# Kernel tuning notes

Measured on AMD Instinct MI355X. Metric: run time of the kernel, lower is better.

## Reference

```python
import jax, jax.numpy as jnp
import numpy as np

B, N, T_IN, F_IN = 16, 30000, 6, 1
E = 120000          # edges per etype
N_ETYPES = 2        # etypes per graph (hg and tg each)
KT, LK = 3, 3
C1, C2 = 8, 11      # block channel sizes
HID = 128


def _conv2d(x, w, b):
    # x: [B,Cin,T,N], w: [Cout,Cin,kt,1] -> valid conv
    y = jax.lax.conv_general_dilated(x, w, window_strides=(1, 1), padding='VALID',
                                     dimension_numbers=('NCHW', 'OIHW', 'NCHW'))
    return y + b[None, :, None, None]


def _glu_tconv(x, w, b, c_out, x_align):
    # TemporalConvLayer with act='GLU'
    xc = _conv2d(x, w, b)
    return (xc[:, :c_out] + x_align) * jax.nn.sigmoid(xc[:, c_out:])


def _hetcheb(X, edges, W, bias):
    # Heterogeneous ChebConv (sum over edge types), lambda_max=2 => L_hat = -D^-1/2 A D^-1/2
    # X: [S,N,Cin], edges: [n_et,2,E] int32, W: [n_et,Lk,Cin,Cout], bias: [n_et,Cout]
    S, n, cin = X.shape
    Lk = W.shape[1]
    Xn = jnp.transpose(X, (1, 0, 2))  # [N,S,Cin]
    out = jnp.zeros((n, S, W.shape[-1]), X.dtype)
    for e in range(edges.shape[0]):
        src, dst = edges[e, 0], edges[e, 1]
        ones = jnp.ones(src.shape, X.dtype)
        deg_in = jnp.clip(jax.ops.segment_sum(ones, dst, num_segments=n), 1.0)
        deg_out = jnp.clip(jax.ops.segment_sum(ones, src, num_segments=n), 1.0)
        norm = jax.lax.rsqrt(deg_out)[src] * jax.lax.rsqrt(deg_in)[dst]  # [E]
        def prop(Tm):  # L_hat @ T = -(Ahat @ T); vectorized over all B*T slices at once
            Tf = Tm.reshape(n, S * cin)
            return -jax.ops.segment_sum(norm[:, None] * Tf[src], dst, num_segments=n).reshape(n, S, cin)
        Tkm2 = Xn
        Tkm1 = prop(Xn)
        z = jnp.einsum('nsc,cd->nsd', Tkm2, W[e, 0]) + jnp.einsum('nsc,cd->nsd', Tkm1, W[e, 1])
        for k in range(2, Lk):
            Tk = 2.0 * prop(Tkm1) - Tkm2
            z = z + jnp.einsum('nsc,cd->nsd', Tk, W[e, k])
            Tkm2, Tkm1 = Tkm1, Tk
        out = out + z + bias[e][None, None, :]
    return jnp.transpose(out, (1, 0, 2))  # [S,N,Cout]


def _block(x, hg_edges, tg_edges, align_fn, tw, tb, hW, hb, tW, tb2, c_out):
    # HetETAConvBlock (dropout = identity in eval)
    x_align = align_fn(x)[:, :, KT - 1:, :]
    x_t1 = _glu_tconv(x, tw, tb, c_out, x_align)          # [B,c_out,T',N]
    b_, c_, t_, n_ = x_t1.shape
    X = jnp.transpose(x_t1, (0, 2, 3, 1)).reshape(b_ * t_, n_, c_)  # batched slices
    xs = _hetcheb(X, hg_edges, hW, hb).reshape(b_, t_, n_, -1).transpose(0, 3, 1, 2)
    xt = _hetcheb(X, tg_edges, tW, tb2).reshape(b_, t_, n_, -1).transpose(0, 3, 1, 2)
    return jnp.concatenate([xs, xt], axis=1)              # [B,2*c_out,T',N]


def setup_inputs() -> dict:
    key = jax.random.key(0)
    ks = jax.random.split(key, 20)
    s = 0.1
    inp = {
        'x': jax.random.normal(ks[0], (B, N, T_IN, F_IN), jnp.float32),
        'hg_edges': jax.random.randint(ks[1], (N_ETYPES, 2, E), 0, N, jnp.int32),
        'tg_edges': jax.random.randint(ks[2], (N_ETYPES, 2, E), 0, N, jnp.int32),
        # block1: tconv GLU 1 -> 8 (out 2*8 channels)
        'tconv1_w': jax.random.normal(ks[3], (2 * C1, F_IN, KT, 1), jnp.float32) * s,
        'tconv1_b': jnp.zeros((2 * C1,), jnp.float32),
        'h1_W': jax.random.normal(ks[4], (N_ETYPES, LK, C1, C1), jnp.float32) * s,
        'h1_b': jnp.zeros((N_ETYPES, C1), jnp.float32),
        't1_W': jax.random.normal(ks[5], (N_ETYPES, LK, C1, C1), jnp.float32) * s,
        't1_b': jnp.zeros((N_ETYPES, C1), jnp.float32),
        # block2: align 16 -> 11 (conv1x1), tconv GLU 16 -> 11
        'align2_w': jax.random.normal(ks[6], (C2, 2 * C1, 1, 1), jnp.float32) * s,
        'align2_b': jnp.zeros((C2,), jnp.float32),
        'tconv2_w': jax.random.normal(ks[7], (2 * C2, 2 * C1, KT, 1), jnp.float32) * s,
        'tconv2_b': jnp.zeros((2 * C2,), jnp.float32),
        'h2_W': jax.random.normal(ks[8], (N_ETYPES, LK, C2, C2), jnp.float32) * s,
        'h2_b': jnp.zeros((N_ETYPES, C2), jnp.float32),
        't2_W': jax.random.normal(ks[9], (N_ETYPES, LK, C2, C2), jnp.float32) * s,
        't2_b': jnp.zeros((N_ETYPES, C2), jnp.float32),
        # output linear: 11*2*(6-2*(3-1)) = 44 -> HID
        'out_w': jax.random.normal(ks[10], (2 * C2 * (T_IN - 2 * (KT - 1)), HID), jnp.float32) * s,
        'out_b': jnp.zeros((HID,), jnp.float32),
    }
    return inp


def reference(x, hg_edges, tg_edges, tconv1_w, tconv1_b, h1_W, h1_b, t1_W, t1_b,
              align2_w, align2_b, tconv2_w, tconv2_b, h2_W, h2_b, t2_W, t2_b,
              out_w, out_b):
    x = jnp.transpose(x, (0, 3, 2, 1))  # [B,1,T,N]
    # block1: Align pads channels 1 -> 8
    align1 = lambda v: jnp.pad(v, ((0, 0), (0, C1 - F_IN), (0, 0), (0, 0)))
    x1 = _block(x, hg_edges, tg_edges, align1, tconv1_w, tconv1_b, h1_W, h1_b, t1_W, t1_b, C1)
    # block2: Align is 1x1 conv 16 -> 11
    align2 = lambda v: _conv2d(v, align2_w, align2_b)
    x2 = _block(x1, hg_edges, tg_edges, align2, tconv2_w, tconv2_b, h2_W, h2_b, t2_W, t2_b, C2)
    b_, c_, t_, n_ = x2.shape
    z = jnp.transpose(x2, (0, 3, 1, 2)).reshape(b_, n_, c_ * t_)  # [B,N,44]
    return z @ out_w + out_b  # [B,N,HID]
```

## Files before the change

### kernel.cpp

```cpp
#include <hip/hip_runtime.h>
#include <hip/hip_fp16.h>
#include <math.h>

#define EDGES 120000
#define NN    30000
#define NCH   118
#define T1SLOT 15360000

__device__ __forceinline__ float sigmoidf_(float x) { return 1.f / (1.f + __expf(-x)); }

union F4H8 { float4 v; __half h[8]; };
union F2H4 { float2 v; __half h[4]; };

__device__ __forceinline__ void unpack8(float4 v, float* f) {
  F4H8 u; u.v = v;
#pragma unroll
  for (int i = 0; i < 8; ++i) f[i] = __half2float(u.h[i]);
}
__device__ __forceinline__ float4 pack8(const float* f) {
  F4H8 u;
#pragma unroll
  for (int i = 0; i < 8; ++i) u.h[i] = __float2half(f[i]);
  return u.v;
}
__device__ __forceinline__ void unpack4(float2 v, float* f) {
  F2H4 u; u.v = v;
#pragma unroll
  for (int i = 0; i < 4; ++i) f[i] = __half2float(u.h[i]);
}
__device__ __forceinline__ float2 pack4(const float* f) {
  F2H4 u;
#pragma unroll
  for (int i = 0; i < 4; ++i) u.h[i] = __float2half(f[i]);
  return u.v;
}

#define CSR_STRIDE 270016
#define CSR_RP(base, l)   ((base) + (size_t)(l) * CSR_STRIDE)
#define CSR_PK(base, l)   ((const int2*)((base) + (size_t)(l) * CSR_STRIDE + 30016))
#define CSR_PKW(base, l)  ((int2*)((base) + (size_t)(l) * CSR_STRIDE + 30016))

__global__ void count_all_kernel(const int* __restrict__ hg, const int* __restrict__ tg,
                                 int* __restrict__ degO, int* __restrict__ degI) {
  int tid = blockIdx.x * blockDim.x + threadIdx.x;
  if (tid >= 4 * EDGES) return;
  int l = tid / EDGES, j = tid - l * EDGES;
  const int* G = (l < 2) ? hg : tg;
  const int* src = G + (size_t)(l & 1) * 2 * EDGES;
  const int* dst = src + EDGES;
  atomicAdd(&degO[l * NN + src[j]], 1);
  atomicAdd(&degI[l * NN + dst[j]], 1);
}

__global__ __launch_bounds__(256) void scan1_kernel(const int* __restrict__ degI,
                                                    int* __restrict__ csrBase,
                                                    int* __restrict__ partials) {
  int l = blockIdx.x / NCH, ch = blockIdx.x - l * NCH;
  int tid = threadIdx.x;
  int i = ch * 256 + tid;
  __shared__ int buf[256];
  int v = (i < NN) ? degI[l * NN + i] : 0;
  buf[tid] = v;
  __syncthreads();
  for (int off = 1; off < 256; off <<= 1) {
    int t = (tid >= off) ? buf[tid - off] : 0;
    __syncthreads();
    buf[tid] += t;
    __syncthreads();
  }
  int* rp = CSR_RP(csrBase, l);
  if (i < NN) rp[i + 1] = buf[tid];
  if (tid == 255) partials[l * NCH + ch] = buf[255];
}

__global__ __launch_bounds__(128) void scan2_kernel(int* __restrict__ partials) {
  __shared__ int buf[128];
  int tid = threadIdx.x;
  for (int l = 0; l < 4; ++l) {
    int v = (tid < NCH) ? partials[l * NCH + tid] : 0;
    buf[tid] = v;
    __syncthreads();
    for (int off = 1; off < 128; off <<= 1) {
      int t = (tid >= off) ? buf[tid - off] : 0;
      __syncthreads();
      buf[tid] += t;
      __syncthreads();
    }
    if (tid < NCH) partials[l * NCH + tid] = buf[tid] - v;
    __syncthreads();
  }
}

__global__ __launch_bounds__(256) void fixup_kernel(int* __restrict__ csrBase,
                                                    int* __restrict__ cursor,
                                                    const int* __restrict__ partials) {
  int l = blockIdx.x / NCH, ch = blockIdx.x - l * NCH;
  int i = ch * 256 + threadIdx.x;
  int* rp = CSR_RP(csrBase, l);
  int off = partials[l * NCH + ch];
  if (i < NN) {
    int val = rp[i + 1] + off;
    rp[i + 1] = val;
    if (i + 1 < NN) cursor[l * NN + i + 1] = val;
  }
  if (i == 0) { rp[0] = 0; cursor[l * NN] = 0; }
}

__global__ void fill_all_kernel(const int* __restrict__ hg, const int* __restrict__ tg,
                                const int* __restrict__ degO, const int* __restrict__ degI,
                                int* __restrict__ cursor, int* __restrict__ csrBase) {
  int tid = blockIdx.x * blockDim.x + threadIdx.x;
  if (tid >= 4 * EDGES) return;
  int l = tid / EDGES, j = tid - l * EDGES;
  const int* G = (l < 2) ? hg : tg;
  const int* src = G + (size_t)(l & 1) * 2 * EDGES;
  const int* dst = src + EDGES;
  int s = src[j], d = dst[j];
  int doo = degO[l * NN + s]; if (doo < 1) doo = 1;
  int dii = degI[l * NN + d]; if (dii < 1) dii = 1;
  float nm = rsqrtf((float)doo) * rsqrtf((float)dii);
  int p = atomicAdd(&cursor[l * NN + d], 1);
  CSR_PKW(csrBase, l)[p] = make_int2(s, __float_as_int(nm));
}

__global__ void glu1_kernel(const float* __restrict__ x, const float* __restrict__ w,
                            const float* __restrict__ b, __half* __restrict__ X1h) {
  int idx = blockIdx.x * blockDim.x + threadIdx.x;
  if (idx >= NN * 64) return;
  int n = idx >> 6, s = idx & 63;
  int bb = s >> 2, t = s & 3;
  const float* xb = x + ((long)bb * NN + n) * 6;
  float x0 = xb[t], x1 = xb[t + 1], x2 = xb[t + 2];
  float o[8];
#pragma unroll
  for (int c = 0; c < 8; ++c) {
    float p = w[c * 3 + 0] * x0 + w[c * 3 + 1] * x1 + w[c * 3 + 2] * x2 + b[c];
    float q = w[(c + 8) * 3 + 0] * x0 + w[(c + 8) * 3 + 1] * x1 + w[(c + 8) * 3 + 2] * x2 + b[c + 8];
    float al = (c == 0) ? x2 : 0.f;
    o[c] = (p + al) * sigmoidf_(q);
  }
  reinterpret_cast<float4*>(X1h)[idx] = pack8(o);
}

__global__ __launch_bounds__(256) void pull1_kernel(const int* __restrict__ csrBase,
                                                    const __half* __restrict__ Xh,
                                                    __half* __restrict__ T1hAll) {
  int gtid = blockIdx.x * 256 + threadIdx.x;
  int l = gtid / (NN * 64);
  int t = gtid - l * (NN * 64);
  int n = t >> 6, j = t & 63;
  const int* rp = CSR_RP(csrBase, l);
  const int2* pk = CSR_PK(csrBase, l);
  const float4* in4 = reinterpret_cast<const float4*>(Xh);
  float acc[8];
#pragma unroll
  for (int i = 0; i < 8; ++i) acc[i] = 0.f;
  int e = rp[n], end = rp[n + 1];
  for (; e + 4 <= end; e += 4) {
    int2 p0 = pk[e], p1 = pk[e + 1], p2 = pk[e + 2], p3 = pk[e + 3];
    float4 v0 = in4[(long)p0.x * 64 + j];
    float4 v1 = in4[(long)p1.x * 64 + j];
    float4 v2 = in4[(long)p2.x * 64 + j];
    float4 v3 = in4[(long)p3.x * 64 + j];
    float f[8];
    float n0 = __int_as_float(p0.y), n1 = __int_as_float(p1.y);
    float n2 = __int_as_float(p2.y), n3 = __int_as_float(p3.y);
    unpack8(v0, f);
#pragma unroll
    for (int i = 0; i < 8; ++i) acc[i] -= n0 * f[i];
    unpack8(v1, f);
#pragma unroll
    for (int i = 0; i < 8; ++i) acc[i] -= n1 * f[i];
    unpack8(v2, f);
#pragma unroll
    for (int i = 0; i < 8; ++i) acc[i] -= n2 * f[i];
    unpack8(v3, f);
#pragma unroll
    for (int i = 0; i < 8; ++i) acc[i] -= n3 * f[i];
  }
  for (; e < end; ++e) {
    int2 p = pk[e];
    float4 v = in4[(long)p.x * 64 + j];
    float nm = __int_as_float(p.y);
    float f[8];
    unpack8(v, f);
#pragma unroll
    for (int i = 0; i < 8; ++i) acc[i] -= nm * f[i];
  }
  reinterpret_cast<float4*>(T1hAll)[(size_t)l * (T1SLOT / 8) + t] = pack8(acc);
}

__global__ __launch_bounds__(256) void cheb1_kernel(const int* __restrict__ csrBase,
    const __half* __restrict__ Xh, const __half* __restrict__ T1hAll,
    const float* __restrict__ Whg, const float* __restrict__ bhg,
    const float* __restrict__ Wtg, const float* __restrict__ btg,
    __half* __restrict__ outH, __half* __restrict__ outT) {
  constexpr int C = 8, CC = 64;
  __shared__ float wx[CC], w1a[CC], w1b[CC], w2a[CC], w2b[CC], bs[C];
  int gtid = blockIdx.x * 256 + threadIdx.x;
  int g = gtid / (NN * 64);
  int tid = gtid - g * (NN * 64);
  const float* W = g ? Wtg : Whg;
  const float* bias = g ? btg : bhg;
  for (int i = threadIdx.x; i < CC; i += 256) {
    float w0A = W[i], w1A = W[CC + i], w2A = W[2 * CC + i];
    float w0B = W[3 * CC + i], w1B = W[4 * CC + i], w2B = W[5 * CC + i];
    wx[i] = w0A - w2A + w0B - w2B;
    w1a[i] = w1A; w1b[i] = w1B;
    w2a[i] = -2.f * w2A; w2b[i] = -2.f * w2B;
  }
  if (threadIdx.x < C) bs[threadIdx.x] = bias[threadIdx.x] + bias[C + threadIdx.x];
  __syncthreads();
  int n = tid >> 6, s = tid & 63;
  int l0 = 2 * g, l1 = 2 * g + 1;
  const int* rp0 = CSR_RP(csrBase, l0); const int2* pk0 = CSR_PK(csrBase, l0);
  const int* rp1 = CSR_RP(csrBase, l1); const int2* pk1 = CSR_PK(csrBase, l1);
  const float4* A4 = reinterpret_cast<const float4*>(T1hAll + (size_t)l0 * T1SLOT);
  const float4* B4 = reinterpret_cast<const float4*>(T1hAll + (size_t)l1 * T1SLOT);
  float acc0[C], acc1[C];
#pragma unroll
  for (int c = 0; c < C; ++c) { acc0[c] = 0.f; acc1[c] = 0.f; }
  {
    int e = rp0[n], end = rp0[n + 1];
    for (; e + 2 <= end; e += 2) {
      int2 p0 = pk0[e], p1 = pk0[e + 1];
      float4 v0 = A4[(long)p0.x * 64 + s];
      float4 v1 = A4[(long)p1.x * 64 + s];
      float n0 = __int_as_float(p0.y), n1 = __int_as_float(p1.y);
      float f0[8], f1[8];
      unpack8(v0, f0); unpack8(v1, f1);
#pragma unroll
      for (int c = 0; c < C; ++c) acc0[c] += n0 * f0[c] + n1 * f1[c];
    }
    for (; e < end; ++e) {
      int2 p = pk0[e];
      float4 v = A4[(long)p.x * 64 + s];
      float nm = __int_as_float(p.y);
      float f[8]; unpack8(v, f);
#pragma unroll
      for (int c = 0; c < C; ++c) acc0[c] += nm * f[c];
    }
  }
  {
    int e = rp1[n], end = rp1[n + 1];
    for (; e + 2 <= end; e += 2) {
      int2 p0 = pk1[e], p1 = pk1[e + 1];
      float4 v0 = B4[(long)p0.x * 64 + s];
      float4 v1 = B4[(long)p1.x * 64 + s];
      float n0 = __int_as_float(p0.y), n1 = __int_as_float(p1.y);
      float f0[8], f1[8];
      unpack8(v0, f0); unpack8(v1, f1);
#pragma unroll
      for (int c = 0; c < C; ++c) acc1[c] += n0 * f0[c] + n1 * f1[c];
    }
    for (; e < end; ++e) {
      int2 p = pk1[e];
      float4 v = B4[(long)p.x * 64 + s];
      float nm = __int_as_float(p.y);
      float f[8]; unpack8(v, f);
#pragma unroll
      for (int c = 0; c < C; ++c) acc1[c] += nm * f[c];
    }
  }
  float z[C];
#pragma unroll
  for (int d = 0; d < C; ++d) z[d] = bs[d];
  {
    float xv[8], av[8], bv[8];
    unpack8(reinterpret_cast<const float4*>(Xh)[tid], xv);
    unpack8(A4[tid], av);
    unpack8(B4[tid], bv);
#pragma unroll
    for (int c = 0; c < C; ++c) {
      float x0c = xv[c], tac = av[c], tbc = bv[c], a0 = acc0[c], a1 = acc1[c];
#pragma unroll
      for (int d = 0; d < C; ++d)
        z[d] += x0c * wx[c * C + d] + tac * w1a[c * C + d] + tbc * w1b[c * C + d] +
                a0 * w2a[c * C + d] + a1 * w2b[c * C + d];
    }
  }
  reinterpret_cast<float4*>(g ? outT : outH)[tid] = pack8(z);
}

__global__ __launch_bounds__(256) void glu2_kernel(const __half* __restrict__ H, const __half* __restrict__ Tt,
                                                   const float* __restrict__ w2, const float* __restrict__ b2,
                                                   const float* __restrict__ aw, const float* __restrict__ ab,
                                                   __half* __restrict__ X2nh) {
  __shared__ float w2s[22 * 16 * 3], b2s[22], aws[11 * 16], abs_[11];
  for (int i = threadIdx.x; i < 22 * 16 * 3; i += 256) w2s[i] = w2[i];
  if (threadIdx.x < 22) b2s[threadIdx.x] = b2[threadIdx.x];
  for (int i = threadIdx.x; i < 11 * 16; i += 256) aws[i] = aw[i];
  if (threadIdx.x < 11) abs_[threadIdx.x] = ab[threadIdx.x];
  __syncthreads();
  int idx = blockIdx.x * 256 + threadIdx.x;
  int n = idx >> 5, s = idx & 31;
  int bb = s >> 1, t = s & 1;
  long rbase = (long)n * 64 + bb * 4 + t;
  const float4* H4 = reinterpret_cast<const float4*>(H) + rbase;
  const float4* T4 = reinterpret_cast<const float4*>(Tt) + rbase;
  float hv[24], tv[24];
  unpack8(H4[0], hv); unpack8(H4[1], hv + 8); unpack8(H4[2], hv + 16);
  unpack8(T4[0], tv); unpack8(T4[1], tv + 8); unpack8(T4[2], tv + 16);
  float o[12];
  o[11] = 0.f;
#pragma unroll
  for (int co = 0; co < 11; ++co) {
    float p = b2s[co], q = b2s[co + 11], a = abs_[co];
#pragma unroll
    for (int ci = 0; ci < 16; ++ci) {
      float v0 = (ci < 8) ? hv[ci] : tv[ci - 8];
      float v1 = (ci < 8) ? hv[8 + ci] : tv[ci];
      float v2 = (ci < 8) ? hv[16 + ci] : tv[8 + ci];
      p += w2s[(co * 16 + ci) * 3 + 0] * v0 + w2s[(co * 16 + ci) * 3 + 1] * v1 +
           w2s[(co * 16 + ci) * 3 + 2] * v2;
      q += w2s[((co + 11) * 16 + ci) * 3 + 0] * v0 + w2s[((co + 11) * 16 + ci) * 3 + 1] * v1 +
           w2s[((co + 11) * 16 + ci) * 3 + 2] * v2;
      a += aws[co * 16 + ci] * v2;
    }
    o[co] = (p + a) * sigmoidf_(q);
  }
  float2* o2 = reinterpret_cast<float2*>(X2nh) + (long)idx * 3;
  o2[0] = pack4(o);
  o2[1] = pack4(o + 4);
  o2[2] = pack4(o + 8);
}

__global__ __launch_bounds__(256) void pull2_kernel(const int* __restrict__ csrBase,
                                                    const __half* __restrict__ Xh,
                                                    __half* __restrict__ T1hAll) {
  int gtid = blockIdx.x * 256 + threadIdx.x;
  int l = gtid / (NN * 96);
  int t = gtid - l * (NN * 96);
  int n = t / 96, j = t - n * 96;
  const int* rp = CSR_RP(csrBase, l);
  const int2* pk = CSR_PK(csrBase, l);
  const float2* in2 = reinterpret_cast<const float2*>(Xh);
  float acc[4];
#pragma unroll
  for (int i = 0; i < 4; ++i) acc[i] = 0.f;
  int e = rp[n], end = rp[n + 1];
  for (; e + 4 <= end; e += 4) {
    int2 p0 = pk[e], p1 = pk[e + 1], p2 = pk[e + 2], p3 = pk[e + 3];
    float2 v0 = in2[(long)p0.x * 96 + j];
    float2 v1 = in2[(long)p1.x * 96 + j];
    float2 v2 = in2[(long)p2.x * 96 + j];
    float2 v3 = in2[(long)p3.x * 96 + j];
    float f[4];
    float n0 = __int_as_float(p0.y), n1 = __int_as_float(p1.y);
    float n2 = __int_as_float(p2.y), n3 = __int_as_float(p3.y);
    unpack4(v0, f);
#pragma unroll
    for (int i = 0; i < 4; ++i) acc[i] -= n0 * f[i];
    unpack4(v1, f);
#pragma unroll
    for (int i = 0; i < 4; ++i) acc[i] -= n1 * f[i];
    unpack4(v2, f);
#pragma unroll
    for (int i = 0; i < 4; ++i) acc[i] -= n2 * f[i];
    unpack4(v3, f);
#pragma unroll
    for (int i = 0; i < 4; ++i) acc[i] -= n3 * f[i];
  }
  for (; e < end; ++e) {
    int2 p = pk[e];
    float2 v = in2[(long)p.x * 96 + j];
    float nm = __int_as_float(p.y);
    float f[4];
    unpack4(v, f);
#pragma unroll
    for (int i = 0; i < 4; ++i) acc[i] -= nm * f[i];
  }
  reinterpret_cast<float2*>(T1hAll)[(size_t)l * (T1SLOT / 4) + t] = pack4(acc);
}

__global__ __launch_bounds__(256) void cheb2_kernel(const int* __restrict__ csrBase,
    const __half* __restrict__ Xh, const __half* __restrict__ T1hAll,
    const float* __restrict__ Whg, const float* __restrict__ bhg,
    const float* __restrict__ Wtg, const float* __restrict__ btg,
    __half* __restrict__ outH, __half* __restrict__ outT) {
  constexpr int C = 11, CC = 121;
  __shared__ float wx[CC], w1a[CC], w1b[CC], w2a[CC], w2b[CC], bs[C];
  int gtid = blockIdx.x * 256 + threadIdx.x;
  int g = gtid / (NN * 32);
  int tid = gtid - g * (NN * 32);
  const float* W = g ? Wtg : Whg;
  const float* bias = g ? btg : bhg;
  for (int i = threadIdx.x; i < CC; i += 256) {
    float w0A = W[i], w1A = W[CC + i], w2A = W[2 * CC + i];
    float w0B = W[3 * CC + i], w1B = W[4 * CC + i], w2B = W[5 * CC + i];
    wx[i] = w0A - w2A + w0B - w2B;
    w1a[i] = w1A; w1b[i] = w1B;
    w2a[i] = -2.f * w2A; w2b[i] = -2.f * w2B;
  }
  if (threadIdx.x < C) bs[threadIdx.x] = bias[threadIdx.x] + bias[C + threadIdx.x];
  __syncthreads();
  int n = tid >> 5, s = tid & 31;
  int s3 = s * 3;
  int l0 = 2 * g, l1 = 2 * g + 1;
  const int* rp0 = CSR_RP(csrBase, l0); const int2* pk0 = CSR_PK(csrBase, l0);
  const int* rp1 = CSR_RP(csrBase, l1); const int2* pk1 = CSR_PK(csrBase, l1);
  const float2* A2v = reinterpret_cast<const float2*>(T1hAll + (size_t)l0 * T1SLOT);
  const float2* B2v = reinterpret_cast<const float2*>(T1hAll + (size_t)l1 * T1SLOT);
// ... 42 lines not shown
      for (int i = 0; i < 4; ++i) acc0[4 + i] += nm * f[i];
      unpack4(a2, f);
#pragma unroll
      for (int i = 0; i < 4; ++i) acc0[8 + i] += nm * f[i];
    }
  }
  {
    int e = rp1[n], end = rp1[n + 1];
    for (; e + 2 <= end; e += 2) {
      int2 p0 = pk1[e], p1 = pk1[e + 1];
      long r0 = (long)p0.x * 96 + s3, r1 = (long)p1.x * 96 + s3;
      float2 a0 = B2v[r0], a1 = B2v[r0 + 1], a2 = B2v[r0 + 2];
      float2 b0 = B2v[r1], b1 = B2v[r1 + 1], b2 = B2v[r1 + 2];
      float n0 = __int_as_float(p0.y), n1 = __int_as_float(p1.y);
      float f[4];
      unpack4(a0, f);
#pragma unroll
      for (int i = 0; i < 4; ++i) acc1[i] += n0 * f[i];
      unpack4(a1, f);
#pragma unroll
      for (int i = 0; i < 4; ++i) acc1[4 + i] += n0 * f[i];
      unpack4(a2, f);
#pragma unroll
      for (int i = 0; i < 4; ++i) acc1[8 + i] += n0 * f[i];
      unpack4(b0, f);
#pragma unroll
      for (int i = 0; i < 4; ++i) acc1[i] += n1 * f[i];
      unpack4(b1, f);
#pragma unroll
      for (int i = 0; i < 4; ++i) acc1[4 + i] += n1 * f[i];
      unpack4(b2, f);
#pragma unroll
      for (int i = 0; i < 4; ++i) acc1[8 + i] += n1 * f[i];
    }
    for (; e < end; ++e) {
      int2 p = pk1[e];
      long r = (long)p.x * 96 + s3;
      float2 a0 = B2v[r], a1 = B2v[r + 1], a2 = B2v[r + 2];
      float nm = __int_as_float(p.y);
      float f[4];
      unpack4(a0, f);
#pragma unroll
      for (int i = 0; i < 4; ++i) acc1[i] += nm * f[i];
      unpack4(a1, f);
#pragma unroll
      for (int i = 0; i < 4; ++i) acc1[4 + i] += nm * f[i];
      unpack4(a2, f);
#pragma unroll
      for (int i = 0; i < 4; ++i) acc1[8 + i] += nm * f[i];
    }
  }
  float z[12];
#pragma unroll
  for (int d = 0; d < C; ++d) z[d] = bs[d];
  z[11] = 0.f;
  const float2* X2v = reinterpret_cast<const float2*>(Xh);
  long own = (long)tid * 3;
#pragma unroll
  for (int q = 0; q < 3; ++q) {
    float xv[4], av[4], bv[4];
    unpack4(X2v[own + q], xv);
    unpack4(A2v[own + q], av);
    unpack4(B2v[own + q], bv);
#pragma unroll
    for (int k = 0; k < 4; ++k) {
      int c = q * 4 + k;
      if (c == 11) continue;
      float x0c = xv[k], tac = av[k], tbc = bv[k], a0 = acc0[c], a1 = acc1[c];
#pragma unroll
      for (int d = 0; d < C; ++d)
        z[d] += x0c * wx[c * C + d] + tac * w1a[c * C + d] + tbc * w1b[c * C + d] +
                a0 * w2a[c * C + d] + a1 * w2b[c * C + d];
    }
  }
  float2* o2 = reinterpret_cast<float2*>(g ? outT : outH) + (long)tid * 3;
  o2[0] = pack4(z);
  o2[1] = pack4(z + 4);
  o2[2] = pack4(z + 8);
}

__global__ __launch_bounds__(256) void final_kernel(const __half* __restrict__ H2, const __half* __restrict__ T2b,
                                                    const float* __restrict__ W, const float* __restrict__ bias,
                                                    float* __restrict__ out) {
  __shared__ __half zsr[64][48];
  int tid = threadIdx.x;
  long r0 = (long)blockIdx.x * 64;
#pragma unroll
  for (int it = 0; it < 2; ++it) {
    int item = it * 256 + tid;
    if (item < 384) {
      int row = item / 6, piece = item - row * 6;
      long r = r0 + row;
      int b = (int)(r / NN), n = (int)(r - (long)b * NN);
      const float4* srcb = reinterpret_cast<const float4*>(piece < 3 ? H2 : T2b);
      int f4i = (piece < 3) ? piece : piece - 3;
      float4 v = srcb[(long)n * 48 + b * 3 + f4i];
      *reinterpret_cast<float4*>(&zsr[row][(piece < 3 ? 0 : 24) + f4i * 8]) = v;
    }
  }
  int c = tid & 127, h = tid >> 7;
  float wp[48];
#pragma unroll
  for (int off = 0; off < 48; ++off) {
    int half_ = off / 24, r_ = off - half_ * 24;
    int t = r_ / 12, c_ = r_ - t * 12;
    wp[off] = (c_ == 11) ? 0.f : W[(2 * (c_ + half_ * 11) + t) * 128 + c];
  }
  float bh = bias[c];
  __syncthreads();
  int rbeg = h * 32;
#pragma unroll 2
  for (int row = rbeg; row < rbeg + 32; ++row) {
    const float4* zr4 = reinterpret_cast<const float4*>(&zsr[row][0]);
    float acc = bh;
#pragma unroll
    for (int q = 0; q < 6; ++q) {
      F4H8 u; u.v = zr4[q];
#pragma unroll
      for (int i = 0; i < 8; ++i)
        acc = fmaf(__half2float(u.h[i]), wp[q * 8 + i], acc);
    }
    out[(r0 + row) * 128 + c] = acc;
  }
}

extern "C" void kernel_launch(void* const* d_in, const int* in_sizes, int n_in,
                              void* d_out, int out_size, void* d_ws, size_t ws_size,
                              hipStream_t stream) {
  const float* x    = (const float*)d_in[0];
  const int*   hg   = (const int*)d_in[1];
  const int*   tg   = (const int*)d_in[2];
  const float* t1w  = (const float*)d_in[3];
  const float* t1b  = (const float*)d_in[4];
  const float* h1W  = (const float*)d_in[5];
  const float* h1b  = (const float*)d_in[6];
  const float* g1W  = (const float*)d_in[7];
  const float* g1b  = (const float*)d_in[8];
  const float* a2w  = (const float*)d_in[9];
  const float* a2b  = (const float*)d_in[10];
  const float* t2w  = (const float*)d_in[11];
  const float* t2b  = (const float*)d_in[12];
  const float* h2W  = (const float*)d_in[13];
  const float* h2b  = (const float*)d_in[14];
  const float* g2W  = (const float*)d_in[15];
  const float* g2b  = (const float*)d_in[16];
  const float* outw = (const float*)d_in[17];
  const float* outb = (const float*)d_in[18];
  float* out = (float*)d_out;

  __half* T1h = (__half*)d_ws;
  __half* Xh  = T1h + 4L * T1SLOT;
  __half* Cfh = Xh + T1SLOT;
  __half* Dfh = Cfh + T1SLOT;
  int* csrBase  = (int*)(Dfh + T1SLOT);
  int* degO     = csrBase + 4 * CSR_STRIDE;
  int* degI     = degO + 4 * NN;
  int* cursor   = degI + 4 * NN;
  int* partials = cursor + 4 * NN;

  hipMemsetAsync(degO, 0, 8 * NN * sizeof(int), stream);
  count_all_kernel<<<(4 * EDGES + 255) / 256, 256, 0, stream>>>(hg, tg, degO, degI);
  scan1_kernel<<<4 * NCH, 256, 0, stream>>>(degI, csrBase, partials);
  scan2_kernel<<<1, 128, 0, stream>>>(partials);
  fixup_kernel<<<4 * NCH, 256, 0, stream>>>(csrBase, cursor, partials);
  fill_all_kernel<<<(4 * EDGES + 255) / 256, 256, 0, stream>>>(hg, tg, degO, degI, cursor, csrBase);

  glu1_kernel<<<NN * 64 / 256, 256, 0, stream>>>(x, t1w, t1b, Xh);
  pull1_kernel<<<4 * NN * 64 / 256, 256, 0, stream>>>(csrBase, Xh, T1h);
  cheb1_kernel<<<2 * NN * 64 / 256, 256, 0, stream>>>(csrBase, Xh, T1h, h1W, h1b, g1W, g1b, Cfh, Dfh);

  glu2_kernel<<<NN * 32 / 256, 256, 0, stream>>>(Cfh, Dfh, t2w, t2b, a2w, a2b, Xh);
  pull2_kernel<<<4 * NN * 96 / 256, 256, 0, stream>>>(csrBase, Xh, T1h);
  cheb2_kernel<<<2 * NN * 32 / 256, 256, 0, stream>>>(csrBase, Xh, T1h, h2W, h2b, g2W, g2b, Cfh, Dfh);

  final_kernel<<<7500, 256, 0, stream>>>(Cfh, Dfh, outw, outb, out);
}
```

Before: 831.1 us.

## Restructure block-1 Chebyshev layout per batch group with XCD-aware persistent scheduling

Changes the block-1 feature layout from node-major [N][B*T][C] to batch-major [B][N][T*C]. Each thread of the pull and cheb kernels now owns one node and one batch, accumulating 32 values per edge over contiguous 64-byte rows. The kernels use persistent blocks that map batches to XCDs (blockIdx & 7) so each XCD's L2 holds the gather source for its batches. Cheb1 now writes per-edge-type partials that glu2 sums, and stores use non-temporal hints. The final kernel becomes grid-stride and the workspace buffers are aliased. The risks are higher register pressure from 32 accumulators, more partial traffic, and reliance on the blockIdx-to-XCD mapping.

```diff
diff --git a/kernel.cpp b/kernel.cpp
--- a/kernel.cpp
+++ b/kernel.cpp
@@ -5,11 +5,13 @@
 #define EDGES 120000
 #define NN    30000
 #define NCH   118
+#define CHUNKS 118
 #define T1SLOT 15360000
 
 __device__ __forceinline__ float sigmoidf_(float x) { return 1.f / (1.f + __expf(-x)); }
 
-union F4H8 { float4 v; __half h[8]; };
+typedef float f4raw __attribute__((ext_vector_type(4)));
+union F4H8 { float4 v; f4raw r; __half h[8]; };
 union F2H4 { float2 v; __half h[4]; };
 
 __device__ __forceinline__ void unpack8(float4 v, float* f) {
@@ -32,6 +34,14 @@
   F2H4 u;
 #pragma unroll
   for (int i = 0; i < 4; ++i) u.h[i] = __float2half(f[i]);
+  return u.v;
+}
+__device__ __forceinline__ void nt_store4(float4* p, float4 v) {
+  F4H8 u; u.v = v;
+  __builtin_nontemporal_store(u.r, reinterpret_cast<f4raw*>(p));
+}
+__device__ __forceinline__ float4 nt_load4(const float4* p) {
+  F4H8 u; u.r = __builtin_nontemporal_load(reinterpret_cast<const f4raw*>(p));
   return u.v;
 }
 
@@ -123,166 +133,201 @@
   CSR_PKW(csrBase, l)[p] = make_int2(s, __float_as_int(nm));
 }
 
-__global__ void glu1_kernel(const float* __restrict__ x, const float* __restrict__ w,
-                            const float* __restrict__ b, __half* __restrict__ X1h) {
-  int idx = blockIdx.x * blockDim.x + threadIdx.x;
-  if (idx >= NN * 64) return;
-  int n = idx >> 6, s = idx & 63;
-  int bb = s >> 2, t = s & 3;
-  const float* xb = x + ((long)bb * NN + n) * 6;
-  float x0 = xb[t], x1 = xb[t + 1], x2 = xb[t + 2];
+__global__ __launch_bounds__(256) void glu1_kernel(const float* __restrict__ x, const float* __restrict__ w,
+                                                   const float* __restrict__ b, __half* __restrict__ X1p) {
+  int tid = blockIdx.x * 256 + threadIdx.x;
+  int q = tid & 3;
+  int gn = tid >> 2;
+  int g = gn / NN, n = gn - g * NN;
+  const float* xb = x + ((long)g * NN + n) * 6;
+  float x0 = xb[q], x1 = xb[q + 1], x2 = xb[q + 2];
   float o[8];
 #pragma unroll
   for (int c = 0; c < 8; ++c) {
     float p = w[c * 3 + 0] * x0 + w[c * 3 + 1] * x1 + w[c * 3 + 2] * x2 + b[c];
-    float q = w[(c + 8) * 3 + 0] * x0 + w[(c + 8) * 3 + 1] * x1 + w[(c + 8) * 3 + 2] * x2 + b[c + 8];
+    float qq = w[(c + 8) * 3 + 0] * x0 + w[(c + 8) * 3 + 1] * x1 + w[(c + 8) * 3 + 2] * x2 + b[c + 8];
     float al = (c == 0) ? x2 : 0.f;
-    o[c] = (p + al) * sigmoidf_(q);
-  }
-  reinterpret_cast<float4*>(X1h)[idx] = pack8(o);
+    o[c] = (p + al) * sigmoidf_(qq);
+  }
+  reinterpret_cast<float4*>(X1p)[tid] = pack8(o);
 }
 
 __global__ __launch_bounds__(256) void pull1_kernel(const int* __restrict__ csrBase,
-                                                    const __half* __restrict__ Xh,
-                                                    __half* __restrict__ T1hAll) {
-  int gtid = blockIdx.x * 256 + threadIdx.x;
-  int l = gtid / (NN * 64);
-  int t = gtid - l * (NN * 64);
-  int n = t >> 6, j = t & 63;
-  const int* rp = CSR_RP(csrBase, l);
-  const int2* pk = CSR_PK(csrBase, l);
-  const float4* in4 = reinterpret_cast<const float4*>(Xh);
-  float acc[8];
-#pragma unroll
-  for (int i = 0; i < 8; ++i) acc[i] = 0.f;
-  int e = rp[n], end = rp[n + 1];
-  for (; e + 4 <= end; e += 4) {
-    int2 p0 = pk[e], p1 = pk[e + 1], p2 = pk[e + 2], p3 = pk[e + 3];
-    float4 v0 = in4[(long)p0.x * 64 + j];
-    float4 v1 = in4[(long)p1.x * 64 + j];
-    float4 v2 = in4[(long)p2.x * 64 + j];
-    float4 v3 = in4[(long)p3.x * 64 + j];
-    float f[8];
-    float n0 = __int_as_float(p0.y), n1 = __int_as_float(p1.y);
-    float n2 = __int_as_float(p2.y), n3 = __int_as_float(p3.y);
-    unpack8(v0, f);
-#pragma unroll
-    for (int i = 0; i < 8; ++i) acc[i] -= n0 * f[i];
-    unpack8(v1, f);
-#pragma unroll
-    for (int i = 0; i < 8; ++i) acc[i] -= n1 * f[i];
-    unpack8(v2, f);
-#pragma unroll
-    for (int i = 0; i < 8; ++i) acc[i] -= n2 * f[i];
-    unpack8(v3, f);
-#pragma unroll
-    for (int i = 0; i < 8; ++i) acc[i] -= n3 * f[i];
-  }
-  for (; e < end; ++e) {
-    int2 p = pk[e];
-    float4 v = in4[(long)p.x * 64 + j];
-    float nm = __int_as_float(p.y);
-    float f[8];
-    unpack8(v, f);
-#pragma unroll
-    for (int i = 0; i < 8; ++i) acc[i] -= nm * f[i];
-  }
-  reinterpret_cast<float4*>(T1hAll)[(size_t)l * (T1SLOT / 8) + t] = pack8(acc);
+                                                    const __half* __restrict__ X1p,
+                                                    __half* __restrict__ T1p) {
+  int xcd = blockIdx.x & 7, bslot = blockIdx.x >> 3;
+  for (int it = bslot; it < 2 * 4 * CHUNKS; it += 256) {
+    int chunk = it % CHUNKS;
+    int li = it / CHUNKS;
+    int l = li & 3, gl = li >> 2;
+    int g = gl * 8 + xcd;
+    int n = chunk * 256 + threadIdx.x;
+    if (n >= NN) continue;
+    const int* rp = CSR_RP(csrBase, l);
+    const int2* pk = CSR_PK(csrBase, l);
+    const float4* Xp = reinterpret_cast<const float4*>(X1p) + (size_t)g * NN * 4;
+    float acc[32];
+#pragma unroll
+    for (int i = 0; i < 32; ++i) acc[i] = 0.f;
+    int e = rp[n], end = rp[n + 1];
+    for (; e + 2 <= end; e += 2) {
+      int2 p0 = pk[e], p1 = pk[e + 1];
+      const float4* r0 = Xp + (size_t)p0.x * 4;
+      const float4* r1 = Xp + (size_t)p1.x * 4;
+      float4 a0 = r0[0], a1 = r0[1], a2 = r0[2], a3 = r0[3];
+      float4 b0 = r1[0], b1 = r1[1], b2 = r1[2], b3 = r1[3];
+      float n0 = __int_as_float(p0.y), n1 = __int_as_float(p1.y);
+      float f[8];
+      unpack8(a0, f);
+#pragma unroll
+      for (int i = 0; i < 8; ++i) acc[i] -= n0 * f[i];
+      unpack8(a1, f);
+#pragma unroll
+      for (int i = 0; i < 8; ++i) acc[8 + i] -= n0 * f[i];
+      unpack8(a2, f);
+#pragma unroll
+      for (int i = 0; i < 8; ++i) acc[16 + i] -= n0 * f[i];
+      unpack8(a3, f);
+#pragma unroll
+      for (int i = 0; i < 8; ++i) acc[24 + i] -= n0 * f[i];
+      unpack8(b0, f);
+#pragma unroll
+      for (int i = 0; i < 8; ++i) acc[i] -= n1 * f[i];
+      unpack8(b1, f);
+#pragma unroll
+      for (int i = 0; i < 8; ++i) acc[8 + i] -= n1 * f[i];
+      unpack8(b2, f);
+#pragma unroll
+      for (int i = 0; i < 8; ++i) acc[16 + i] -= n1 * f[i];
+      unpack8(b3, f);
+#pragma unroll
+      for (int i = 0; i < 8; ++i) acc[24 + i] -= n1 * f[i];
+    }
+    for (; e < end; ++e) {
+      int2 p = pk[e];
+      const float4* r0 = Xp + (size_t)p.x * 4;
+      float nm = __int_as_float(p.y);
+      float f[8];
+#pragma unroll
+      for (int rqi = 0; rqi < 4; ++rqi) {
+        unpack8(r0[rqi], f);
+#pragma unroll
+        for (int i = 0; i < 8; ++i) acc[rqi * 8 + i] -= nm * f[i];
+      }
+    }
+    float4* dst = reinterpret_cast<float4*>(T1p) + ((size_t)(l * 16 + g) * NN + n) * 4;
+    nt_store4(dst + 0, pack8(acc));
+    nt_store4(dst + 1, pack8(acc + 8));
+    nt_store4(dst + 2, pack8(acc + 16));
+    nt_store4(dst + 3, pack8(acc + 24));
+  }
 }
 
 __global__ __launch_bounds__(256) void cheb1_kernel(const int* __restrict__ csrBase,
-    const __half* __restrict__ Xh, const __half* __restrict__ T1hAll,
+    const __half* __restrict__ X1p, const __half* __restrict__ T1p,
     const float* __restrict__ Whg, const float* __restrict__ bhg,
     const float* __restrict__ Wtg, const float* __restrict__ btg,
-    __half* __restrict__ outH, __half* __restrict__ outT) {
-  constexpr int C = 8, CC = 64;
-  __shared__ float wx[CC], w1a[CC], w1b[CC], w2a[CC], w2b[CC], bs[C];
-  int gtid = blockIdx.x * 256 + threadIdx.x;
-  int g = gtid / (NN * 64);
-  int tid = gtid - g * (NN * 64);
-  const float* W = g ? Wtg : Whg;
-  const float* bias = g ? btg : bhg;
-  for (int i = threadIdx.x; i < CC; i += 256) {
-    float w0A = W[i], w1A = W[CC + i], w2A = W[2 * CC + i];
-    float w0B = W[3 * CC + i], w1B = W[4 * CC + i], w2B = W[5 * CC + i];
-    wx[i] = w0A - w2A + w0B - w2B;
-    w1a[i] = w1A; w1b[i] = w1B;
-    w2a[i] = -2.f * w2A; w2b[i] = -2.f * w2B;
-  }
-  if (threadIdx.x < C) bs[threadIdx.x] = bias[threadIdx.x] + bias[C + threadIdx.x];
-  __syncthreads();
-  int n = tid >> 6, s = tid & 63;
-  int l0 = 2 * g, l1 = 2 * g + 1;
-  const int* rp0 = CSR_RP(csrBase, l0); const int2* pk0 = CSR_PK(csrBase, l0);
-  const int* rp1 = CSR_RP(csrBase, l1); const int2* pk1 = CSR_PK(csrBase, l1);
-  const float4* A4 = reinterpret_cast<const float4*>(T1hAll + (size_t)l0 * T1SLOT);
-  const float4* B4 = reinterpret_cast<const float4*>(T1hAll + (size_t)l1 * T1SLOT);
-  float acc0[C], acc1[C];
-#pragma unroll
-  for (int c = 0; c < C; ++c) { acc0[c] = 0.f; acc1[c] = 0.f; }
-  {
-    int e = rp0[n], end = rp0[n + 1];
+    __half* __restrict__ P1) {
+  __shared__ float wx[64], w1[64], w2[64], bs[8];
+  int xcd = blockIdx.x & 7, bslot = blockIdx.x >> 3;
+  for (int it = bslot; it < 2 * 4 * CHUNKS; it += 256) {
+    int chunk = it % CHUNKS;
+    int li = it / CHUNKS;
+    int l = li & 3, gl = li >> 2;
+    int g = gl * 8 + xcd;
+    __syncthreads();
+    {
+      int grf = l >> 1, et = l & 1;
+      const float* W = (grf ? Wtg : Whg) + et * 3 * 64;
+      const float* bias = (grf ? btg : bhg) + et * 8;
+      for (int i = threadIdx.x; i < 64; i += 256) {
+        float w0v = W[i], w1v = W[64 + i], w2v = W[128 + i];
+        wx[i] = w0v - w2v; w1[i] = w1v; w2[i] = -2.f * w2v;
+      }
+      if (threadIdx.x < 8) bs[threadIdx.x] = bias[threadIdx.x];
+    }
+    __syncthreads();
+    int n = chunk * 256 + threadIdx.x;
+    if (n >= NN) continue;
+    const int* rp = CSR_RP(csrBase, l);
+    const int2* pk = CSR_PK(csrBase, l);
+    const float4* Tp = reinterpret_cast<const float4*>(T1p) + (size_t)(l * 16 + g) * NN * 4;
+    float acc[32];
+#pragma unroll
+    for (int i = 0; i < 32; ++i) acc[i] = 0.f;
+    int e = rp[n], end = rp[n + 1];
     for (; e + 2 <= end; e += 2) {
-      int2 p0 = pk0[e], p1 = pk0[e + 1];
-      float4 v0 = A4[(long)p0.x * 64 + s];
-      float4 v1 = A4[(long)p1.x * 64 + s];
+      int2 p0 = pk[e], p1 = pk[e + 1];
+      const float4* r0 = Tp + (size_t)p0.x * 4;
+      const float4* r1 = Tp + (size_t)p1.x * 4;
+      float4 a0 = r0[0], a1 = r0[1], a2 = r0[2], a3 = r0[3];
+      float4 b0 = r1[0], b1 = r1[1], b2 = r1[2], b3 = r1[3];
       float n0 = __int_as_float(p0.y), n1 = __int_as_float(p1.y);
-      float f0[8], f1[8];
-      unpack8(v0, f0); unpack8(v1, f1);
-#pragma unroll
-      for (int c = 0; c < C; ++c) acc0[c] += n0 * f0[c] + n1 * f1[c];
+      float f[8];
+      unpack8(a0, f);
+#pragma unroll
+      for (int i = 0; i < 8; ++i) acc[i] += n0 * f[i];
+      unpack8(a1, f);
+#pragma unroll
+      for (int i = 0; i < 8; ++i) acc[8 + i] += n0 * f[i];
+      unpack8(a2, f);
+#pragma unroll
+      for (int i = 0; i < 8; ++i) acc[16 + i] += n0 * f[i];
+      unpack8(a3, f);
+#pragma unroll
+      for (int i = 0; i < 8; ++i) acc[24 + i] += n0 * f[i];
+      unpack8(b0, f);
+#pragma unroll
+      for (int i = 0; i < 8; ++i) acc[i] += n1 * f[i];
+      unpack8(b1, f);
+#pragma unroll
+      for (int i = 0; i < 8; ++i) acc[8 + i] += n1 * f[i];
+      unpack8(b2, f);
+#pragma unroll
+      for (int i = 0; i < 8; ++i) acc[16 + i] += n1 * f[i];
+      unpack8(b3, f);
+#pragma unroll
+      for (int i = 0; i < 8; ++i) acc[24 + i] += n1 * f[i];
     }
     for (; e < end; ++e) {
-      int2 p = pk0[e];
-      float4 v = A4[(long)p.x * 64 + s];
+      int2 p = pk[e];
+      const float4* r0 = Tp + (size_t)p.x * 4;
       float nm = __int_as_float(p.y);
-      float f[8]; unpack8(v, f);
-#pragma unroll
-      for (int c = 0; c < C; ++c) acc0[c] += nm * f[c];
-    }
-  }
-  {
-    int e = rp1[n], end = rp1[n + 1];
-    for (; e + 2 <= end; e += 2) {
-      int2 p0 = pk1[e], p1 = pk1[e + 1];
-      float4 v0 = B4[(long)p0.x * 64 + s];
-      float4 v1 = B4[(long)p1.x * 64 + s];
-      float n0 = __int_as_float(p0.y), n1 = __int_as_float(p1.y);
-      float f0[8], f1[8];
-      unpack8(v0, f0); unpack8(v1, f1);
-#pragma unroll
-      for (int c = 0; c < C; ++c) acc1[c] += n0 * f0[c] + n1 * f1[c];
-    }
-    for (; e < end; ++e) {
-      int2 p = pk1[e];
-      float4 v = B4[(long)p.x * 64 + s];
-      float nm = __int_as_float(p.y);
-      float f[8]; unpack8(v, f);
-#pragma unroll
-      for (int c = 0; c < C; ++c) acc1[c] += nm * f[c];
-    }
-  }
-  float z[C];
-#pragma unroll
-  for (int d = 0; d < C; ++d) z[d] = bs[d];
-  {
-    float xv[8], av[8], bv[8];
-    unpack8(reinterpret_cast<const float4*>(Xh)[tid], xv);
-    unpack8(A4[tid], av);
-    unpack8(B4[tid], bv);
-#pragma unroll
-    for (int c = 0; c < C; ++c) {
-      float x0c = xv[c], tac = av[c], tbc = bv[c], a0 = acc0[c], a1 = acc1[c];
-#pragma unroll
-      for (int d = 0; d < C; ++d)
-        z[d] += x0c * wx[c * C + d] + tac * w1a[c * C + d] + tbc * w1b[c * C + d] +
-                a0 * w2a[c * C + d] + a1 * w2b[c * C + d];
-    }
-  }
-  reinterpret_cast<float4*>(g ? outT : outH)[tid] = pack8(z);
-}
-
-__global__ __launch_bounds__(256) void glu2_kernel(const __half* __restrict__ H, const __half* __restrict__ Tt,
+      float f[8];
+#pragma unroll
+      for (int rqi = 0; rqi < 4; ++rqi) {
+        unpack8(r0[rqi], f);
+#pragma unroll
+        for (int i = 0; i < 8; ++i) acc[rqi * 8 + i] += nm * f[i];
+      }
+    }
+    const float4* Xr = reinterpret_cast<const float4*>(X1p) + ((size_t)g * NN + n) * 4;
+    float4 xr[4];
+#pragma unroll
+    for (int qd = 0; qd < 4; ++qd) xr[qd] = nt_load4(Xr + qd);
+    const float4* Tr = Tp + (size_t)n * 4;
+    float4* dst = reinterpret_cast<float4*>(P1) + ((size_t)(l * 16 + g) * NN + n) * 4;
+#pragma unroll
+    for (int qd = 0; qd < 4; ++qd) {
+      float xv[8], tv[8];
+      unpack8(xr[qd], xv);
+      unpack8(Tr[qd], tv);
+      float z[8];
+#pragma unroll
+      for (int d = 0; d < 8; ++d) z[d] = bs[d];
+#pragma unroll
+      for (int c = 0; c < 8; ++c) {
+        float xc = xv[c], tc = tv[c], ac = acc[qd * 8 + c];
+#pragma unroll
+        for (int d = 0; d < 8; ++d)
+          z[d] += xc * wx[c * 8 + d] + tc * w1[c * 8 + d] + ac * w2[c * 8 + d];
+      }
+      nt_store4(dst + qd, pack8(z));
+    }
+  }
+}
+
+__global__ __launch_bounds__(256) void glu2_kernel(const __half* __restrict__ P1,
                                                    const float* __restrict__ w2, const float* __restrict__ b2,
                                                    const float* __restrict__ aw, const float* __restrict__ ab,
                                                    __half* __restrict__ X2nh) {
@@ -293,14 +338,25 @@
   if (threadIdx.x < 11) abs_[threadIdx.x] = ab[threadIdx.x];
   __syncthreads();
   int idx = blockIdx.x * 256 + threadIdx.x;
-  int n = idx >> 5, s = idx & 31;
-  int bb = s >> 1, t = s & 1;
-  long rbase = (long)n * 64 + bb * 4 + t;
-  const float4* H4 = reinterpret_cast<const float4*>(H) + rbase;
-  const float4* T4 = reinterpret_cast<const float4*>(Tt) + rbase;
-  float hv[24], tv[24];
-  unpack8(H4[0], hv); unpack8(H4[1], hv + 8); unpack8(H4[2], hv + 16);
-  unpack8(T4[0], tv); unpack8(T4[1], tv + 8); unpack8(T4[2], tv + 16);
+  int n = idx >> 5, s2 = idx & 31;
+  int b = s2 >> 1, t = s2 & 1;
+  const float4* P4 = reinterpret_cast<const float4*>(P1);
+  size_t base0 = ((size_t)(0 * 16 + b) * NN + n) * 4 + t;
+  size_t base1 = ((size_t)(1 * 16 + b) * NN + n) * 4 + t;
+  size_t base2 = ((size_t)(2 * 16 + b) * NN + n) * 4 + t;
+  size_t base3 = ((size_t)(3 * 16 + b) * NN + n) * 4 + t;
+  float hv[24], tv[24], tmp[8];
+#pragma unroll
+  for (int k = 0; k < 3; ++k) {
+    unpack8(P4[base0 + k], hv + 8 * k);
+    unpack8(P4[base1 + k], tmp);
+#pragma unroll
+    for (int i = 0; i < 8; ++i) hv[8 * k + i] += tmp[i];
+    unpack8(P4[base2 + k], tv + 8 * k);
+    unpack8(P4[base3 + k], tmp);
+#pragma unroll
+    for (int i = 0; i < 8; ++i) tv[8 * k + i] += tmp[i];
+  }
   float o[12];
   o[11] = 0.f;
 #pragma unroll
@@ -528,20 +584,6 @@
                                                     float* __restrict__ out) {
   __shared__ __half zsr[64][48];
   int tid = threadIdx.x;
-  long r0 = (long)blockIdx.x * 64;
-#pragma unroll
-  for (int it = 0; it < 2; ++it) {
-    int item = it * 256 + tid;
-    if (item < 384) {
-      int row = item / 6, piece = item - row * 6;
-      long r = r0 + row;
-      int b = (int)(r / NN), n = (int)(r - (long)b * NN);
-      const float4* srcb = reinterpret_cast<const float4*>(piece < 3 ? H2 : T2b);
-      int f4i = (piece < 3) ? piece : piece - 3;
-      float4 v = srcb[(long)n * 48 + b * 3 + f4i];
-      *reinterpret_cast<float4*>(&zsr[row][(piece < 3 ? 0 : 24) + f4i * 8]) = v;
-    }
-  }
   int c = tid & 127, h = tid >> 7;
   float wp[48];
 #pragma unroll
@@ -551,20 +593,37 @@
     wp[off] = (c_ == 11) ? 0.f : W[(2 * (c_ + half_ * 11) + t) * 128 + c];
   }
   float bh = bias[c];
-  __syncthreads();
-  int rbeg = h * 32;
+  for (int tile = blockIdx.x; tile < 7500; tile += gridDim.x) {
+    long r0 = (long)tile * 64;
+    __syncthreads();
+#pragma unroll
+    for (int it = 0; it < 2; ++it) {
+      int item = it * 256 + tid;
+      if (item < 384) {
+        int row = item / 6, piece = item - row * 6;
+        long r = r0 + row;
+        int b = (int)(r / NN), n = (int)(r - (long)b * NN);
+        const float4* srcb = reinterpret_cast<const float4*>(piece < 3 ? H2 : T2b);
+        int f4i = (piece < 3) ? piece : piece - 3;
+        float4 v = srcb[(long)n * 48 + b * 3 + f4i];
+        *reinterpret_cast<float4*>(&zsr[row][(piece < 3 ? 0 : 24) + f4i * 8]) = v;
+      }
+    }
+    __syncthreads();
+    int rbeg = h * 32;
 #pragma unroll 2
-  for (int row = rbeg; row < rbeg + 32; ++row) {
-    const float4* zr4 = reinterpret_cast<const float4*>(&zsr[row][0]);
-    float acc = bh;
-#pragma unroll
-    for (int q = 0; q < 6; ++q) {
-      F4H8 u; u.v = zr4[q];
-#pragma unroll
-      for (int i = 0; i < 8; ++i)
-        acc = fmaf(__half2float(u.h[i]), wp[q * 8 + i], acc);
-    }
-    out[(r0 + row) * 128 + c] = acc;
+    for (int row = rbeg; row < rbeg + 32; ++row) {
+      const float4* zr4 = reinterpret_cast<const float4*>(&zsr[row][0]);
+      float acc = bh;
+#pragma unroll
+      for (int q = 0; q < 6; ++q) {
+        F4H8 u; u.v = zr4[q];
+#pragma unroll
+        for (int i = 0; i < 8; ++i)
+          acc = fmaf(__half2float(u.h[i]), wp[q * 8 + i], acc);
+      }
+      out[(r0 + row) * 128 + c] = acc;
+    }
   }
 }
 
@@ -592,12 +651,15 @@
   const float* outb = (const float*)d_in[18];
   float* out = (float*)d_out;
 
-  __half* T1h = (__half*)d_ws;
-  __half* Xh  = T1h + 4L * T1SLOT;
-  __half* Cfh = Xh + T1SLOT;
-  __half* Dfh = Cfh + T1SLOT;
-  int* csrBase  = (int*)(Dfh + T1SLOT);
-  int* degO     = csrBase + 4 * CSR_STRIDE;
+  __half* T1p  = (__half*)d_ws;
+  __half* Cfh  = T1p;
+  __half* Dfh  = T1p + 11520000;
+  __half* X1p  = T1p + 4L * T1SLOT;
+  __half* X2nh = X1p;
+  __half* P1   = X1p + T1SLOT;
+  __half* T1h2 = P1;
+  int* csrBase  = (int*)(P1 + 4L * T1SLOT);
+  int* degO     = (int*)P1;
   int* degI     = degO + 4 * NN;
   int* cursor   = degI + 4 * NN;
   int* partials = cursor + 4 * NN;
@@ -609,13 +671,13 @@
   fixup_kernel<<<4 * NCH, 256, 0, stream>>>(csrBase, cursor, partials);
   fill_all_kernel<<<(4 * EDGES + 255) / 256, 256, 0, stream>>>(hg, tg, degO, degI, cursor, csrBase);
 
-  glu1_kernel<<<NN * 64 / 256, 256, 0, stream>>>(x, t1w, t1b, Xh);
-  pull1_kernel<<<4 * NN * 64 / 256, 256, 0, stream>>>(csrBase, Xh, T1h);
-  cheb1_kernel<<<2 * NN * 64 / 256, 256, 0, stream>>>(csrBase, Xh, T1h, h1W, h1b, g1W, g1b, Cfh, Dfh);
-
-  glu2_kernel<<<NN * 32 / 256, 256, 0, stream>>>(Cfh, Dfh, t2w, t2b, a2w, a2b, Xh);
-  pull2_kernel<<<4 * NN * 96 / 256, 256, 0, stream>>>(csrBase, Xh, T1h);
-  cheb2_kernel<<<2 * NN * 32 / 256, 256, 0, stream>>>(csrBase, Xh, T1h, h2W, h2b, g2W, g2b, Cfh, Dfh);
-
-  final_kernel<<<7500, 256, 0, stream>>>(Cfh, Dfh, outw, outb, out);
-}
+  glu1_kernel<<<16 * NN * 4 / 256, 256, 0, stream>>>(x, t1w, t1b, X1p);
+  pull1_kernel<<<2048, 256, 0, stream>>>(csrBase, X1p, T1p);
+  cheb1_kernel<<<2048, 256, 0, stream>>>(csrBase, X1p, T1p, h1W, h1b, g1W, g1b, P1);
+
+  glu2_kernel<<<NN * 32 / 256, 256, 0, stream>>>(P1, t2w, t2b, a2w, a2b, X2nh);
+  pull2_kernel<<<4 * NN * 96 / 256, 256, 0, stream>>>(csrBase, X2nh, T1h2);
+  cheb2_kernel<<<2 * NN * 32 / 256, 256, 0, stream>>>(csrBase, X2nh, T1h2, h2W, h2b, g2W, g2b, Cfh, Dfh);
+
+  final_kernel<<<1024, 256, 0, stream>>>(Cfh, Dfh, outw, outb, out);
+}
```

Measured after the change: 1.331 ms. 60.1% more time.

## Restructure glu2 weights for vectorized LDS reads and make final kernel persistent

Applied to the files above, without the earlier changes.

glu2 now pre-transposes the temporal-conv and align weights in shared memory into a [tap*ci][co] layout padded to 24 and 12 columns. Each input value then does float4 broadcast reads and FMAs into 24+12 accumulators instead of scalar strided lookups. The final projection kernel becomes grid-stride persistent over 1024 blocks, so the per-column weight registers are loaded once per block and reused across many tiles. It also stores the staged rows as fp32 in LDS, removing the per-row half-to-float conversion. The trade-off is more registers in glu2 and double the LDS footprint in the final kernel.

```diff
diff --git a/kernel.cpp b/kernel.cpp
--- a/kernel.cpp
+++ b/kernel.cpp
@@ -282,15 +282,24 @@
   reinterpret_cast<float4*>(g ? outT : outH)[tid] = pack8(z);
 }
 
-__global__ __launch_bounds__(256) void glu2_kernel(const __half* __restrict__ H, const __half* __restrict__ Tt,
-                                                   const float* __restrict__ w2, const float* __restrict__ b2,
-                                                   const float* __restrict__ aw, const float* __restrict__ ab,
-                                                   __half* __restrict__ X2nh) {
-  __shared__ float w2s[22 * 16 * 3], b2s[22], aws[11 * 16], abs_[11];
-  for (int i = threadIdx.x; i < 22 * 16 * 3; i += 256) w2s[i] = w2[i];
-  if (threadIdx.x < 22) b2s[threadIdx.x] = b2[threadIdx.x];
-  for (int i = threadIdx.x; i < 11 * 16; i += 256) aws[i] = aw[i];
-  if (threadIdx.x < 11) abs_[threadIdx.x] = ab[threadIdx.x];
+__global__ __launch_bounds__(256, 4) void glu2_kernel(const __half* __restrict__ H, const __half* __restrict__ Tt,
+                                                      const float* __restrict__ w2, const float* __restrict__ b2,
+                                                      const float* __restrict__ aw, const float* __restrict__ ab,
+                                                      __half* __restrict__ X2nh) {
+  __shared__ float wpq[48 * 24];
+  __shared__ float awl[16 * 12];
+  __shared__ float bpq[22], bal[11];
+  for (int i = threadIdx.x; i < 48 * 24; i += 256) {
+    int k = i / 24, co = i - (i / 24) * 24;
+    int tap = k >> 4, ci = k & 15;
+    wpq[i] = (co < 22) ? w2[(co * 16 + ci) * 3 + tap] : 0.f;
+  }
+  for (int i = threadIdx.x; i < 16 * 12; i += 256) {
+    int ci = i / 12, co = i - ci * 12;
+    awl[i] = (co < 11) ? aw[co * 16 + ci] : 0.f;
+  }
+  if (threadIdx.x < 22) bpq[threadIdx.x] = b2[threadIdx.x];
+  if (threadIdx.x < 11) bal[threadIdx.x] = ab[threadIdx.x];
   __syncthreads();
   int idx = blockIdx.x * 256 + threadIdx.x;
   int n = idx >> 5, s = idx & 31;
@@ -298,26 +307,52 @@
   long rbase = (long)n * 64 + bb * 4 + t;
   const float4* H4 = reinterpret_cast<const float4*>(H) + rbase;
   const float4* T4 = reinterpret_cast<const float4*>(Tt) + rbase;
-  float hv[24], tv[24];
-  unpack8(H4[0], hv); unpack8(H4[1], hv + 8); unpack8(H4[2], hv + 16);
-  unpack8(T4[0], tv); unpack8(T4[1], tv + 8); unpack8(T4[2], tv + 16);
+  float acc[24];
+  float aac[12];
+#pragma unroll
+  for (int i = 0; i < 24; ++i) acc[i] = 0.f;
+#pragma unroll
+  for (int i = 0; i < 12; ++i) aac[i] = 0.f;
+#pragma unroll
+  for (int tap = 0; tap < 3; ++tap) {
+    float hv8[8], tv8[8];
+    unpack8(H4[tap], hv8);
+    unpack8(T4[tap], tv8);
+#pragma unroll
+    for (int half_ = 0; half_ < 2; ++half_) {
+#pragma unroll
+      for (int c8 = 0; c8 < 8; ++c8) {
+        float v = half_ ? tv8[c8] : hv8[c8];
+        const float4* w4 = reinterpret_cast<const float4*>(&wpq[(tap * 16 + half_ * 8 + c8) * 24]);
+#pragma unroll
+        for (int j = 0; j < 6; ++j) {
+          float4 wv = w4[j];
+          acc[4 * j + 0] = fmaf(v, wv.x, acc[4 * j + 0]);
+          acc[4 * j + 1] = fmaf(v, wv.y, acc[4 * j + 1]);
+          acc[4 * j + 2] = fmaf(v, wv.z, acc[4 * j + 2]);
+          acc[4 * j + 3] = fmaf(v, wv.w, acc[4 * j + 3]);
+        }
+        if (tap == 2) {
+          const float4* a4 = reinterpret_cast<const float4*>(&awl[(half_ * 8 + c8) * 12]);
+#pragma unroll
+          for (int j = 0; j < 3; ++j) {
+            float4 wv = a4[j];
+            aac[4 * j + 0] = fmaf(v, wv.x, aac[4 * j + 0]);
+            aac[4 * j + 1] = fmaf(v, wv.y, aac[4 * j + 1]);
+            aac[4 * j + 2] = fmaf(v, wv.z, aac[4 * j + 2]);
+            aac[4 * j + 3] = fmaf(v, wv.w, aac[4 * j + 3]);
+          }
+        }
+      }
+    }
+  }
   float o[12];
   o[11] = 0.f;
 #pragma unroll
   for (int co = 0; co < 11; ++co) {
-    float p = b2s[co], q = b2s[co + 11], a = abs_[co];
-#pragma unroll
-    for (int ci = 0; ci < 16; ++ci) {
-      float v0 = (ci < 8) ? hv[ci] : tv[ci - 8];
-      float v1 = (ci < 8) ? hv[8 + ci] : tv[ci];
-      float v2 = (ci < 8) ? hv[16 + ci] : tv[8 + ci];
-      p += w2s[(co * 16 + ci) * 3 + 0] * v0 + w2s[(co * 16 + ci) * 3 + 1] * v1 +
-           w2s[(co * 16 + ci) * 3 + 2] * v2;
-      q += w2s[((co + 11) * 16 + ci) * 3 + 0] * v0 + w2s[((co + 11) * 16 + ci) * 3 + 1] * v1 +
-           w2s[((co + 11) * 16 + ci) * 3 + 2] * v2;
-      a += aws[co * 16 + ci] * v2;
-    }
-    o[co] = (p + a) * sigmoidf_(q);
+    float p = acc[co] + bpq[co] + aac[co] + bal[co];
+    float q = acc[co + 11] + bpq[co + 11];
+    o[co] = p * sigmoidf_(q);
   }
   float2* o2 = reinterpret_cast<float2*>(X2nh) + (long)idx * 3;
   o2[0] = pack4(o);
@@ -526,22 +561,8 @@
 __global__ __launch_bounds__(256) void final_kernel(const __half* __restrict__ H2, const __half* __restrict__ T2b,
                                                     const float* __restrict__ W, const float* __restrict__ bias,
                                                     float* __restrict__ out) {
-  __shared__ __half zsr[64][48];
+  __shared__ float zsr[64][48];
   int tid = threadIdx.x;
-  long r0 = (long)blockIdx.x * 64;
-#pragma unroll
-  for (int it = 0; it < 2; ++it) {
-    int item = it * 256 + tid;
-    if (item < 384) {
-      int row = item / 6, piece = item - row * 6;
-      long r = r0 + row;
-      int b = (int)(r / NN), n = (int)(r - (long)b * NN);
-      const float4* srcb = reinterpret_cast<const float4*>(piece < 3 ? H2 : T2b);
-      int f4i = (piece < 3) ? piece : piece - 3;
-      float4 v = srcb[(long)n * 48 + b * 3 + f4i];
-      *reinterpret_cast<float4*>(&zsr[row][(piece < 3 ? 0 : 24) + f4i * 8]) = v;
-    }
-  }
   int c = tid & 127, h = tid >> 7;
   float wp[48];
 #pragma unroll
@@ -551,20 +572,42 @@
     wp[off] = (c_ == 11) ? 0.f : W[(2 * (c_ + half_ * 11) + t) * 128 + c];
   }
   float bh = bias[c];
-  __syncthreads();
-  int rbeg = h * 32;
+  for (int tile = blockIdx.x; tile < 7500; tile += gridDim.x) {
+    long r0 = (long)tile * 64;
+    __syncthreads();
+#pragma unroll
+    for (int it = 0; it < 2; ++it) {
+      int item = it * 256 + tid;
+      if (item < 384) {
+        int row = item / 6, piece = item - row * 6;
+        long r = r0 + row;
+        int b = (int)(r / NN), n = (int)(r - (long)b * NN);
+        const float4* srcb = reinterpret_cast<const float4*>(piece < 3 ? H2 : T2b);
+        int f4i = (piece < 3) ? piece : piece - 3;
+        float4 v = srcb[(long)n * 48 + b * 3 + f4i];
+        float f[8];
+        unpack8(v, f);
+        float4* d = reinterpret_cast<float4*>(&zsr[row][(piece < 3 ? 0 : 24) + f4i * 8]);
+        d[0] = make_float4(f[0], f[1], f[2], f[3]);
+        d[1] = make_float4(f[4], f[5], f[6], f[7]);
+      }
+    }
+    __syncthreads();
+    int rbeg = h * 32;
 #pragma unroll 2
-  for (int row = rbeg; row < rbeg + 32; ++row) {
-    const float4* zr4 = reinterpret_cast<const float4*>(&zsr[row][0]);
-    float acc = bh;
-#pragma unroll
-    for (int q = 0; q < 6; ++q) {
-      F4H8 u; u.v = zr4[q];
-#pragma unroll
-      for (int i = 0; i < 8; ++i)
-        acc = fmaf(__half2float(u.h[i]), wp[q * 8 + i], acc);
-    }
-    out[(r0 + row) * 128 + c] = acc;
+    for (int row = rbeg; row < rbeg + 32; ++row) {
+      const float4* zr4 = reinterpret_cast<const float4*>(&zsr[row][0]);
+      float acc = bh;
+#pragma unroll
+      for (int q = 0; q < 12; ++q) {
+        float4 zv = zr4[q];
+        acc = fmaf(zv.x, wp[4 * q + 0], acc);
+        acc = fmaf(zv.y, wp[4 * q + 1], acc);
+        acc = fmaf(zv.z, wp[4 * q + 2], acc);
+        acc = fmaf(zv.w, wp[4 * q + 3], acc);
+      }
+      out[(r0 + row) * 128 + c] = acc;
+    }
   }
 }
 
@@ -617,5 +660,5 @@
   pull2_kernel<<<4 * NN * 96 / 256, 256, 0, stream>>>(csrBase, Xh, T1h);
   cheb2_kernel<<<2 * NN * 32 / 256, 256, 0, stream>>>(csrBase, Xh, T1h, h2W, h2b, g2W, g2b, Cfh, Dfh);
 
-  final_kernel<<<7500, 256, 0, stream>>>(Cfh, Dfh, outw, outb, out);
-}
+  final_kernel<<<1024, 256, 0, stream>>>(Cfh, Dfh, outw, outb, out);
+}
```

New measurement: 1.392 ms. +67.5%, slower.
